# Optimization experiments

Measured on AMD Instinct MI355X. Metric: run time of the kernel, lower is better.

The kernel has to match this reference:

```python
import jax, jax.numpy as jnp
import numpy as np

# Collage decoder constants (from init_kwargs)
RES = 256          # config.data_res
C = 3              # collage_width
RH = RW = 8        # range patch size
DH = DW = 64       # domain patch size
N_DH = RES // DH   # 4 domain patches per side
N_D = N_DH * N_DH  # 16 domain patches
N_RH = RES // RH   # 32 range patches per side
N_R = N_RH * N_RH  # 1024 range patches
HF = DH // RH      # 8: pooling factor domain->range size
STEPS = 10


def setup_inputs() -> dict:
    key = jax.random.key(0)
    k1, k2, k3 = jax.random.split(key, 3)
    patch_emb = jax.random.normal(k1, (8, RH, RW, 256), dtype=jnp.float32)
    # get_1x1(theta_width): 1x1 conv == channel matmul, weight (256, 147456)
    w_theta = jax.random.normal(k2, (256, N_R * 3 * N_D * C), dtype=jnp.float32) * 0.01
    b_theta = jax.random.normal(k3, (N_R * 3 * N_D * C,), dtype=jnp.float32) * 0.01
    return {"patch_emb": patch_emb, "w_theta": w_theta, "b_theta": b_theta}


def reference(patch_emb, w_theta, b_theta):
    bs = patch_emb.shape[0]
    # patch_to_theta (1x1 conv) then avg_pool over full spatial extent -> (bs, theta_width)
    theta = jnp.einsum('bhwk,kt->bhwt', patch_emb, w_theta) + b_theta
    theta = theta.mean(axis=(1, 2))
    theta = theta.reshape(bs, 3 * N_R, N_D, C)
    mul, add, mix = jnp.split(theta, 3, axis=1)       # each (bs, N_R, N_D, C)
    mix = jax.nn.softmax(mix, axis=1)                 # softmax over range-patch axis (axis=1)
    mul = jnp.tanh(mul) * mix
    add = jnp.tanh(add) * mix
    add_sum = add.sum(axis=2)                         # (bs, N_R, C)

    iterate = jnp.zeros((bs, RES, RES, C), dtype=patch_emb.dtype)
    for _ in range(STEPS):
        # partition_img: gather domain patches -> (bs, N_D, DH, DW, C)
        d = iterate.reshape(bs, N_DH, DH, N_DH, DW, C)
        d = d.transpose(0, 1, 3, 2, 4, 5).reshape(bs, N_D, DH, DW, C)
        # reduce: mean-pool each domain patch down to range size (bs, N_D, RH, RW, C)
        d = d.reshape(bs, N_D, RH, HF, RW, HF, C).mean(axis=(3, 5))
        # affine combine: soft collage links every range to every domain
        out = jnp.einsum('brdc,bdhwc->brhwc', mul, d) + add_sum[:, :, None, None, :]
        iterate = out.reshape(bs, N_RH, N_RH, RH, RW, C)
        iterate = iterate.transpose(0, 1, 3, 2, 4, 5).reshape(bs, RES, RES, C)
    return iterate
```

## Files before the change

kernel.cpp:

```cpp
#include <hip/hip_runtime.h>
#include <math.h>

#define T_COLS 147456
#define BS 8
#define NU 49152

#define OFF_ME      0
#define OFF_THETA   2048
#define OFF_MULP    (OFF_THETA + BS*T_COLS)
#define OFF_ADDSUM  (OFF_MULP + 8*3*1024*16)
#define OFF_Q       (OFF_ADDSUM + 8*3*1024)

__device__ __forceinline__ float tanh_fast(float x) {
    float e = __expf(2.f * x);
    return 1.f - 2.f * __builtin_amdgcn_rcpf(e + 1.f);
}

__global__ __launch_bounds__(1024) void k1_mean(const float* __restrict__ pe,
                                                float* __restrict__ me) {
    int b = blockIdx.x;
    int k = threadIdx.x & 255, qd = threadIdx.x >> 8;
    const float* p = pe + (size_t)b * 16384 + qd * 4096 + k;
    float s = 0.f;
#pragma unroll
    for (int i = 0; i < 16; i++) s += p[i * 256];
    __shared__ float part[4][256];
    part[qd][k] = s;
    __syncthreads();
    if (threadIdx.x < 256) {
        float v = part[0][k] + part[1][k] + part[2][k] + part[3][k];
        me[k * 8 + b] = v * (1.f / 64.f);
    }
}

__global__ __launch_bounds__(192) void k2_gemm(const float* __restrict__ w,
                                               const float* __restrict__ bt,
                                               const float* __restrict__ me,
                                               float* __restrict__ tt) {
    __shared__ __align__(16) float lme[2048];
    __shared__ float lt[8][192];
    int tid = threadIdx.x;
    for (int i = tid; i < 2048; i += 192) lme[i] = me[i];
    __syncthreads();

    int t = blockIdx.x * 192 + tid;
    const float* wp = w + t;
    float bv = bt[t];

    float acc[8];
#pragma unroll
    for (int b = 0; b < 8; b++) acc[b] = 0.f;

#pragma unroll 32
    for (int k = 0; k < 256; k++) {
        float wv = wp[(size_t)k * T_COLS];
        const float4* m4 = reinterpret_cast<const float4*>(&lme[k * 8]);
        float4 m0 = m4[0], m1 = m4[1];
        acc[0] += m0.x * wv;
        acc[1] += m0.y * wv;
        acc[2] += m0.z * wv;
        acc[3] += m0.w * wv;
        acc[4] += m1.x * wv;
        acc[5] += m1.y * wv;
        acc[6] += m1.z * wv;
        acc[7] += m1.w * wv;
    }
#pragma unroll
    for (int b = 0; b < 8; b++) lt[b][tid] = acc[b] + bv;
    __syncthreads();

    int u0 = blockIdx.x * 64;
    int j = tid & 63;
    int c = tid >> 6;
#pragma unroll
    for (int b = 0; b < 8; b++) {
        float v = lt[b][j * 3 + c];
        tt[(size_t)(b * 3 + c) * NU + u0 + j] = v;
    }
}

#define MVL_STRIDE 1028
__global__ __launch_bounds__(1024) void kC(const float* __restrict__ tt,
                                           float* __restrict__ mulp,
                                           float* __restrict__ addsum,
                                           float* __restrict__ q) {
    int bc = blockIdx.x;
    int r = threadIdx.x;
    int lane = r & 63, wv = r >> 6;
    const float4* base = reinterpret_cast<const float4*>(tt + (size_t)bc * NU);

    __shared__ float redm[16 * 16];
    __shared__ float gm[16], ginv[16];
    __shared__ float mvl[16 * MVL_STRIDE];
    __shared__ float sred[1024];
    __shared__ float Ash[256];
    __shared__ float svl[16], pl[16];

    float mx[16];
    {
        float4 x0 = base[8192 + r * 4 + 0];
        float4 x1 = base[8192 + r * 4 + 1];
        float4 x2 = base[8192 + r * 4 + 2];
        float4 x3 = base[8192 + r * 4 + 3];
        mx[0] = x0.x; mx[1] = x0.y; mx[2] = x0.z; mx[3] = x0.w;
        mx[4] = x1.x; mx[5] = x1.y; mx[6] = x1.z; mx[7] = x1.w;
        mx[8] = x2.x; mx[9] = x2.y; mx[10] = x2.z; mx[11] = x2.w;
        mx[12] = x3.x; mx[13] = x3.y; mx[14] = x3.z; mx[15] = x3.w;
    }
    {
        float wred[16];
#pragma unroll
        for (int d = 0; d < 16; d++) wred[d] = mx[d];
#pragma unroll
        for (int m = 32; m > 0; m >>= 1)
#pragma unroll
            for (int d = 0; d < 16; d++)
                wred[d] = fmaxf(wred[d], __shfl_xor(wred[d], m));
        if (lane == 0) {
#pragma unroll
            for (int d = 0; d < 16; d++) redm[wv * 16 + d] = wred[d];
        }
    }
    __syncthreads();
    if (r < 16) {
        float m = -1e30f;
#pragma unroll
        for (int w = 0; w < 16; w++) m = fmaxf(m, redm[w * 16 + r]);
        gm[r] = m;
    }
    __syncthreads();

    {
        float wred[16];
#pragma unroll
        for (int d = 0; d < 16; d++) {
            mx[d] = __expf(mx[d] - gm[d]);
            wred[d] = mx[d];
        }
#pragma unroll
        for (int m = 32; m > 0; m >>= 1)
#pragma unroll
            for (int d = 0; d < 16; d++)
                wred[d] += __shfl_xor(wred[d], m);
        if (lane == 0) {
#pragma unroll
            for (int d = 0; d < 16; d++) redm[wv * 16 + d] = wred[d];
        }
    }
    __syncthreads();
    if (r < 16) {
        float s = 0.f;
#pragma unroll
        for (int w = 0; w < 16; w++) s += redm[w * 16 + r];
        ginv[r] = 1.f / s;
    }
    __syncthreads();
#pragma unroll
    for (int d = 0; d < 16; d++) mx[d] *= ginv[d];

    float asum = 0.f;
    {
        float4 a0 = base[4096 + r * 4 + 0];
        float4 a1 = base[4096 + r * 4 + 1];
        float4 a2 = base[4096 + r * 4 + 2];
        float4 a3 = base[4096 + r * 4 + 3];
        float av[16];
        av[0] = a0.x; av[1] = a0.y; av[2] = a0.z; av[3] = a0.w;
        av[4] = a1.x; av[5] = a1.y; av[6] = a1.z; av[7] = a1.w;
        av[8] = a2.x; av[9] = a2.y; av[10] = a2.z; av[11] = a2.w;
        av[12] = a3.x; av[13] = a3.y; av[14] = a3.z; av[15] = a3.w;
#pragma unroll
        for (int d = 0; d < 16; d++) asum += tanh_fast(av[d]) * mx[d];
    }
    addsum[(size_t)bc * 1024 + r] = asum;
    sred[r] = asum;

    float mv[16];
    {
        float4 m0 = base[r * 4 + 0];
        float4 m1 = base[r * 4 + 1];
        float4 m2 = base[r * 4 + 2];
        float4 m3 = base[r * 4 + 3];
        mv[0] = m0.x; mv[1] = m0.y; mv[2] = m0.z; mv[3] = m0.w;
        mv[4] = m1.x; mv[5] = m1.y; mv[6] = m1.z; mv[7] = m1.w;
        mv[8] = m2.x; mv[9] = m2.y; mv[10] = m2.z; mv[11] = m2.w;
        mv[12] = m3.x; mv[13] = m3.y; mv[14] = m3.z; mv[15] = m3.w;
#pragma unroll
        for (int d = 0; d < 16; d++) mv[d] = tanh_fast(mv[d]) * mx[d];
    }
    {
        float4* mp = reinterpret_cast<float4*>(&mulp[((size_t)bc * 1024 + r) * 16]);
        mp[0] = make_float4(mv[0], mv[1], mv[2], mv[3]);
        mp[1] = make_float4(mv[4], mv[5], mv[6], mv[7]);
        mp[2] = make_float4(mv[8], mv[9], mv[10], mv[11]);
        mp[3] = make_float4(mv[12], mv[13], mv[14], mv[15]);
    }
#pragma unroll
    for (int d = 0; d < 16; d++) mvl[d * MVL_STRIDE + r] = mv[d];
    __syncthreads();

    if (r < 256) {
        int dd = r >> 4, d = r & 15;
        int di = dd >> 2, dj = dd & 3;
        const float* bse = &mvl[d * MVL_STRIDE + di * 256 + dj * 8];
        float s = 0.f;
        for (int a = 0; a < 8; a++) {
#pragma unroll
            for (int e = 0; e < 8; e++) s += bse[a * 32 + e];
        }
        Ash[r] = s * (1.f / 64.f);
    }
    if (r < 16) {
        int di = r >> 2, dj = r & 3;
        float s = 0.f;
        for (int a = 0; a < 8; a++)
#pragma unroll
            for (int e = 0; e < 8; e++) s += sred[di * 256 + a * 32 + dj * 8 + e];
        svl[r] = s * (1.f / 64.f);
    }
    __syncthreads();

    if (r < 64) {
        int d2 = r & 15;
        float arow[16];
#pragma unroll
        for (int d = 0; d < 16; d++) arow[d] = Ash[d2 * 16 + d];
        float sv = svl[d2];
        float pd = 0.f;
        for (int it = 0; it < 8; it++) {
            float x = sv;
#pragma unroll
            for (int d = 0; d < 16; d++) x += arow[d] * __shfl(pd, d, 16);
            pd = x;
        }
        if (r < 16) pl[r] = pd;
    }
    __syncthreads();

    {
        float x = asum;
#pragma unroll
        for (int d = 0; d < 16; d++) x += mv[d] * pl[d];
        q[(size_t)bc * 1024 + r] = x;
    }
}

__global__ __launch_bounds__(512) void k5_final(const float* __restrict__ mulp,
                                                const float* __restrict__ addsum,
                                                const float* __restrict__ q,
                                                float* __restrict__ out) {
    int blk = blockIdx.x;
    int b = blk >> 5, ri = blk & 31;
    int tid = threadIdx.x;
    __shared__ float ql[3072];
    for (int i = tid; i < 3072; i += 512) ql[i] = q[(size_t)b * 3072 + i];
    __syncthreads();

    int h = tid >> 6;
    int rj = (tid >> 1) & 31;
    int wh = tid & 1;
    int r = ri * 32 + rj;

    float mr[3][16];
    float as[3];
#pragma unroll
    for (int c = 0; c < 3; c++) {
        const float4* mp4 = reinterpret_cast<const float4*>(
            &mulp[((size_t)(b * 3 + c) * 1024 + r) * 16]);
        float4 v0 = mp4[0], v1 = mp4[1], v2 = mp4[2], v3 = mp4[3];
        mr[c][0] = v0.x; mr[c][1] = v0.y; mr[c][2] = v0.z; mr[c][3] = v0.w;
        mr[c][4] = v1.x; mr[c][5] = v1.y; mr[c][6] = v1.z; mr[c][7] = v1.w;
        mr[c][8] = v2.x; mr[c][9] = v2.y; mr[c][10] = v2.z; mr[c][11] = v2.w;
        mr[c][12] = v3.x; mr[c][13] = v3.y; mr[c][14] = v3.z; mr[c][15] = v3.w;
        as[c] = addsum[(size_t)(b * 3 + c) * 1024 + r];
    }

    float acc[3][4];
#pragma unroll
    for (int c = 0; c < 3; c++)
#pragma unroll
        for (int w = 0; w < 4; w++) acc[c][w] = as[c];

#pragma unroll
    for (int di = 0; di < 4; di++) {
        int qrow = (di * 8 + h) * 32;
#pragma unroll
        for (int dj = 0; dj < 4; dj++) {
#pragma unroll
            for (int c = 0; c < 3; c++) {
                float m = mr[c][di * 4 + dj];
                const float* qb = &ql[c * 1024 + qrow + dj * 8 + wh * 4];
                acc[c][0] += m * qb[0];
                acc[c][1] += m * qb[1];
                acc[c][2] += m * qb[2];
                acc[c][3] += m * qb[3];
            }
        }
    }

    int i = ri * 8 + h;
    int j0 = rj * 8 + wh * 4;
    float4* ob = reinterpret_cast<float4*>(
        &out[((size_t)(b * 256 + i) * 256 + j0) * 3]);
    ob[0] = make_float4(acc[0][0], acc[1][0], acc[2][0], acc[0][1]);
    ob[1] = make_float4(acc[1][1], acc[2][1], acc[0][2], acc[1][2]);
    ob[2] = make_float4(acc[2][2], acc[0][3], acc[1][3], acc[2][3]);
}

extern "C" void kernel_launch(void* const* d_in, const int* in_sizes, int n_in,
                              void* d_out, int out_size, void* d_ws, size_t ws_size,
                              hipStream_t stream) {
    const float* pe = (const float*)d_in[0];
    const float* w  = (const float*)d_in[1];
    const float* bt = (const float*)d_in[2];
    float* ws = (float*)d_ws;

    float* me     = ws + OFF_ME;
    float* tt     = ws + OFF_THETA;
    float* mulp   = ws + OFF_MULP;
    float* addsum = ws + OFF_ADDSUM;
    float* q      = ws + OFF_Q;
    float* out = (float*)d_out;

    k1_mean<<<8, 1024, 0, stream>>>(pe, me);
    k2_gemm<<<T_COLS / 192, 192, 0, stream>>>(w, bt, me, tt);
    kC<<<24, 1024, 0, stream>>>(tt, mulp, addsum, q);
    k5_final<<<256, 512, 0, stream>>>(mulp, addsum, q, out);
}
```

Before: 60.77 us.

## Fuse GEMM, softmax and final stages into one persistent kernel with grid barriers

Replaces the three launches after the mean kernel with a single persistent kernel of 768 blocks. Atomic-counter grid barriers separate the theta GEMM, the per-channel softmax/fixed-point stage (now 256 threads handling 4 rows each) and the final image assembly. The aim is to remove kernel launch gaps and tail effects between the stages. The risks are spin-wait cost, a deadlock if 768 blocks are not all co-resident (checked only through an occupancy query), and the middle stage running on just 24 blocks while the rest idle.

```diff
diff --git a/kernel.cpp b/kernel.cpp
--- a/kernel.cpp
+++ b/kernel.cpp
@@ -2,22 +2,35 @@
 #include <math.h>
 
 #define T_COLS 147456
-#define BS 8
 #define NU 49152
 
 #define OFF_ME      0
 #define OFF_THETA   2048
-#define OFF_MULP    (OFF_THETA + BS*T_COLS)
+#define OFF_MULP    (OFF_THETA + 8*T_COLS)
 #define OFF_ADDSUM  (OFF_MULP + 8*3*1024*16)
 #define OFF_Q       (OFF_ADDSUM + 8*3*1024)
+#define OFF_BAR     (OFF_Q + 8*3*1024)
 
 __device__ __forceinline__ float tanh_fast(float x) {
     float e = __expf(2.f * x);
     return 1.f - 2.f * __builtin_amdgcn_rcpf(e + 1.f);
 }
 
-__global__ __launch_bounds__(1024) void k1_mean(const float* __restrict__ pe,
-                                                float* __restrict__ me) {
+__device__ __forceinline__ void gridbar(unsigned int* bar, unsigned int target) {
+    __syncthreads();
+    if (threadIdx.x == 0) {
+        __threadfence();
+        atomicAdd(bar, 1u);
+        while (atomicAdd(bar, 0u) < target) __builtin_amdgcn_s_sleep(2);
+        __threadfence();
+    }
+    __syncthreads();
+}
+
+__global__ __launch_bounds__(1024) void k1z(const float* __restrict__ pe,
+                                            float* __restrict__ me,
+                                            unsigned int* __restrict__ bar) {
+    if (blockIdx.x == 0 && threadIdx.x < 2) bar[threadIdx.x] = 0u;
     int b = blockIdx.x;
     int k = threadIdx.x & 255, qd = threadIdx.x >> 8;
     const float* p = pe + (size_t)b * 16384 + qd * 4096 + k;
@@ -30,6 +43,276 @@
     if (threadIdx.x < 256) {
         float v = part[0][k] + part[1][k] + part[2][k] + part[3][k];
         me[k * 8 + b] = v * (1.f / 64.f);
+    }
+}
+
+__global__ __launch_bounds__(256, 3) void mega(
+        const float* __restrict__ w, const float* __restrict__ bt,
+        const float* __restrict__ me, float* __restrict__ tt,
+        float* __restrict__ mulp, float* __restrict__ addsum,
+        float* __restrict__ q, float* __restrict__ out,
+        unsigned int* __restrict__ bar) {
+    const int bid = blockIdx.x;
+    const int tid = threadIdx.x;
+
+    __shared__ __align__(16) float lme[2048];
+    __shared__ float lt[8][192];
+    __shared__ __align__(16) float red[256 * 16];
+    __shared__ float sred[256];
+    __shared__ float Ash[256];
+    __shared__ float gmax[16], ginv[16], svl[16], pl[16];
+    __shared__ float ql3[3072];
+
+    {
+        for (int i = tid; i < 2048; i += 256) lme[i] = me[i];
+        __syncthreads();
+        if (tid < 192) {
+            int t = bid * 192 + tid;
+            const float* wp = w + t;
+            float acc[8];
+#pragma unroll
+            for (int b = 0; b < 8; b++) acc[b] = 0.f;
+#pragma unroll 16
+            for (int k = 0; k < 256; k++) {
+                float wv = wp[(size_t)k * T_COLS];
+                const float4* m4 = reinterpret_cast<const float4*>(&lme[k * 8]);
+                float4 m0 = m4[0], m1 = m4[1];
+                acc[0] += m0.x * wv; acc[1] += m0.y * wv;
+                acc[2] += m0.z * wv; acc[3] += m0.w * wv;
+                acc[4] += m1.x * wv; acc[5] += m1.y * wv;
+                acc[6] += m1.z * wv; acc[7] += m1.w * wv;
+            }
+            float bv = bt[t];
+#pragma unroll
+            for (int b = 0; b < 8; b++) lt[b][tid] = acc[b] + bv;
+        }
+        __syncthreads();
+        if (tid < 192) {
+            int u0 = bid * 64;
+            int j = tid & 63;
+            int c = tid >> 6;
+#pragma unroll
+            for (int b = 0; b < 8; b++)
+                tt[(size_t)(b * 3 + c) * NU + u0 + j] = lt[b][j * 3 + c];
+        }
+    }
+    gridbar(&bar[0], 768);
+
+    if (bid < 24) {
+        const int bc = bid;
+        const float4* base4 = reinterpret_cast<const float4*>(tt + (size_t)bc * NU);
+        const int r0 = tid * 4;
+        const int lane = tid & 63, wvi = tid >> 6;
+
+        float sm[4][16];
+        float lmax[16];
+#pragma unroll
+        for (int d = 0; d < 16; d++) lmax[d] = -1e30f;
+#pragma unroll
+        for (int i = 0; i < 4; i++) {
+            float4 x0 = base4[(2048 + r0 + i) * 4 + 0];
+            float4 x1 = base4[(2048 + r0 + i) * 4 + 1];
+            float4 x2 = base4[(2048 + r0 + i) * 4 + 2];
+            float4 x3 = base4[(2048 + r0 + i) * 4 + 3];
+            sm[i][0] = x0.x; sm[i][1] = x0.y; sm[i][2] = x0.z; sm[i][3] = x0.w;
+            sm[i][4] = x1.x; sm[i][5] = x1.y; sm[i][6] = x1.z; sm[i][7] = x1.w;
+            sm[i][8] = x2.x; sm[i][9] = x2.y; sm[i][10] = x2.z; sm[i][11] = x2.w;
+            sm[i][12] = x3.x; sm[i][13] = x3.y; sm[i][14] = x3.z; sm[i][15] = x3.w;
+#pragma unroll
+            for (int d = 0; d < 16; d++) lmax[d] = fmaxf(lmax[d], sm[i][d]);
+        }
+#pragma unroll
+        for (int m = 32; m > 0; m >>= 1)
+#pragma unroll
+            for (int d = 0; d < 16; d++)
+                lmax[d] = fmaxf(lmax[d], __shfl_xor(lmax[d], m));
+        if (lane == 0) {
+#pragma unroll
+            for (int d = 0; d < 16; d++) red[wvi * 16 + d] = lmax[d];
+        }
+        __syncthreads();
+        if (tid < 16)
+            gmax[tid] = fmaxf(fmaxf(red[tid], red[16 + tid]),
+                              fmaxf(red[32 + tid], red[48 + tid]));
+        __syncthreads();
+
+        float lsum[16];
+#pragma unroll
+        for (int d = 0; d < 16; d++) lsum[d] = 0.f;
+#pragma unroll
+        for (int i = 0; i < 4; i++)
+#pragma unroll
+            for (int d = 0; d < 16; d++) {
+                sm[i][d] = __expf(sm[i][d] - gmax[d]);
+                lsum[d] += sm[i][d];
+            }
+#pragma unroll
+        for (int m = 32; m > 0; m >>= 1)
+#pragma unroll
+            for (int d = 0; d < 16; d++) lsum[d] += __shfl_xor(lsum[d], m);
+        if (lane == 0) {
+#pragma unroll
+            for (int d = 0; d < 16; d++) red[wvi * 16 + d] = lsum[d];
+        }
+        __syncthreads();
+        if (tid < 16)
+            ginv[tid] = 1.f / (red[tid] + red[16 + tid] + red[32 + tid] + red[48 + tid]);
+        __syncthreads();
+#pragma unroll
+        for (int i = 0; i < 4; i++)
+#pragma unroll
+            for (int d = 0; d < 16; d++) sm[i][d] *= ginv[d];
+
+        float asum[4];
+#pragma unroll
+        for (int i = 0; i < 4; i++) {
+            float4 a0 = base4[(1024 + r0 + i) * 4 + 0];
+            float4 a1 = base4[(1024 + r0 + i) * 4 + 1];
+            float4 a2 = base4[(1024 + r0 + i) * 4 + 2];
+            float4 a3 = base4[(1024 + r0 + i) * 4 + 3];
+            float av[16];
+            av[0] = a0.x; av[1] = a0.y; av[2] = a0.z; av[3] = a0.w;
+            av[4] = a1.x; av[5] = a1.y; av[6] = a1.z; av[7] = a1.w;
+            av[8] = a2.x; av[9] = a2.y; av[10] = a2.z; av[11] = a2.w;
+            av[12] = a3.x; av[13] = a3.y; av[14] = a3.z; av[15] = a3.w;
+            float s = 0.f;
+#pragma unroll
+            for (int d = 0; d < 16; d++) s += tanh_fast(av[d]) * sm[i][d];
+            asum[i] = s;
+            addsum[(size_t)bc * 1024 + r0 + i] = s;
+        }
+        sred[tid] = asum[0] + asum[1] + asum[2] + asum[3];
+
+#pragma unroll
+        for (int i = 0; i < 4; i++) {
+            float4 m0 = base4[(r0 + i) * 4 + 0];
+            float4 m1 = base4[(r0 + i) * 4 + 1];
+            float4 m2 = base4[(r0 + i) * 4 + 2];
+            float4 m3 = base4[(r0 + i) * 4 + 3];
+            float mvv[16];
+            mvv[0] = m0.x; mvv[1] = m0.y; mvv[2] = m0.z; mvv[3] = m0.w;
+            mvv[4] = m1.x; mvv[5] = m1.y; mvv[6] = m1.z; mvv[7] = m1.w;
+            mvv[8] = m2.x; mvv[9] = m2.y; mvv[10] = m2.z; mvv[11] = m2.w;
+            mvv[12] = m3.x; mvv[13] = m3.y; mvv[14] = m3.z; mvv[15] = m3.w;
+#pragma unroll
+            for (int d = 0; d < 16; d++) sm[i][d] = tanh_fast(mvv[d]) * sm[i][d];
+            float4* mp = reinterpret_cast<float4*>(&mulp[((size_t)bc * 1024 + r0 + i) * 16]);
+            mp[0] = make_float4(sm[i][0], sm[i][1], sm[i][2], sm[i][3]);
+            mp[1] = make_float4(sm[i][4], sm[i][5], sm[i][6], sm[i][7]);
+            mp[2] = make_float4(sm[i][8], sm[i][9], sm[i][10], sm[i][11]);
+            mp[3] = make_float4(sm[i][12], sm[i][13], sm[i][14], sm[i][15]);
+        }
+
+#pragma unroll
+        for (int d = 0; d < 16; d++)
+            red[tid * 16 + d] = sm[0][d] + sm[1][d] + sm[2][d] + sm[3][d];
+        __syncthreads();
+        {
+            int dd = tid >> 4, d = tid & 15;
+            int di = dd >> 2, dj = dd & 3;
+            float s = 0.f;
+#pragma unroll
+            for (int a = 0; a < 8; a++) {
+                int t0 = di * 64 + a * 8 + dj * 2;
+                s += red[t0 * 16 + d] + red[(t0 + 1) * 16 + d];
+            }
+            Ash[tid] = s * (1.f / 64.f);
+        }
+        if (tid < 16) {
+            int di = tid >> 2, dj = tid & 3;
+            float s = 0.f;
+#pragma unroll
+            for (int a = 0; a < 8; a++) {
+                int t0 = di * 64 + a * 8 + dj * 2;
+                s += sred[t0] + sred[t0 + 1];
+            }
+            svl[tid] = s * (1.f / 64.f);
+        }
+        __syncthreads();
+
+        if (tid < 64) {
+            int d2 = tid & 15;
+            float arow[16];
+#pragma unroll
+            for (int d = 0; d < 16; d++) arow[d] = Ash[d2 * 16 + d];
+            float sv = svl[d2];
+            float pd = 0.f;
+            for (int it = 0; it < 8; it++) {
+                float x = sv;
+#pragma unroll
+                for (int d = 0; d < 16; d++) x += arow[d] * __shfl(pd, d, 16);
+                pd = x;
+            }
+            if (tid < 16) pl[tid] = pd;
+        }
+        __syncthreads();
+
+#pragma unroll
+        for (int i = 0; i < 4; i++) {
+            float x = asum[i];
+#pragma unroll
+            for (int d = 0; d < 16; d++) x += sm[i][d] * pl[d];
+            q[(size_t)bc * 1024 + r0 + i] = x;
+        }
+    }
+    gridbar(&bar[1], 768);
+
+    if (bid < 256) {
+        int b = bid >> 5, ri = bid & 31;
+        for (int i = tid; i < 3072; i += 256) ql3[i] = q[(size_t)b * 3072 + i];
+        __syncthreads();
+
+        int h0 = tid >> 6;
+        int rj = (tid >> 1) & 31;
+        int wh = tid & 1;
+        int r = ri * 32 + rj;
+
+        float mr[3][16];
+        float as[3];
+#pragma unroll
+        for (int c = 0; c < 3; c++) {
+            const float4* mp4 = reinterpret_cast<const float4*>(
+                &mulp[((size_t)(b * 3 + c) * 1024 + r) * 16]);
+            float4 v0 = mp4[0], v1 = mp4[1], v2 = mp4[2], v3 = mp4[3];
+            mr[c][0] = v0.x; mr[c][1] = v0.y; mr[c][2] = v0.z; mr[c][3] = v0.w;
+            mr[c][4] = v1.x; mr[c][5] = v1.y; mr[c][6] = v1.z; mr[c][7] = v1.w;
+            mr[c][8] = v2.x; mr[c][9] = v2.y; mr[c][10] = v2.z; mr[c][11] = v2.w;
+            mr[c][12] = v3.x; mr[c][13] = v3.y; mr[c][14] = v3.z; mr[c][15] = v3.w;
+            as[c] = addsum[(size_t)(b * 3 + c) * 1024 + r];
+        }
+
+#pragma unroll
+        for (int hh = 0; hh < 2; hh++) {
+            int h = h0 + hh * 4;
+            float acc[3][4];
+#pragma unroll
+            for (int c = 0; c < 3; c++)
+#pragma unroll
+                for (int x = 0; x < 4; x++) acc[c][x] = as[c];
+#pragma unroll
+            for (int di = 0; di < 4; di++) {
+                int qrow = (di * 8 + h) * 32;
+#pragma unroll
+                for (int dj = 0; dj < 4; dj++) {
+#pragma unroll
+                    for (int c = 0; c < 3; c++) {
+                        float m = mr[c][di * 4 + dj];
+                        const float* qb = &ql3[c * 1024 + qrow + dj * 8 + wh * 4];
+                        acc[c][0] += m * qb[0];
+                        acc[c][1] += m * qb[1];
+                        acc[c][2] += m * qb[2];
+                        acc[c][3] += m * qb[3];
+                    }
+                }
+            }
+            int i = ri * 8 + h;
+            int j0 = rj * 8 + wh * 4;
+            float4* ob = reinterpret_cast<float4*>(
+                &out[((size_t)(b * 256 + i) * 256 + j0) * 3]);
+            ob[0] = make_float4(acc[0][0], acc[1][0], acc[2][0], acc[0][1]);
+            ob[1] = make_float4(acc[1][1], acc[2][1], acc[0][2], acc[1][2]);
+            ob[2] = make_float4(acc[2][2], acc[0][3], acc[1][3], acc[2][3]);
+        }
     }
 }
 
@@ -42,41 +325,31 @@
     int tid = threadIdx.x;
     for (int i = tid; i < 2048; i += 192) lme[i] = me[i];
     __syncthreads();
-
     int t = blockIdx.x * 192 + tid;
     const float* wp = w + t;
     float bv = bt[t];
-
     float acc[8];
 #pragma unroll
     for (int b = 0; b < 8; b++) acc[b] = 0.f;
-
 #pragma unroll 32
     for (int k = 0; k < 256; k++) {
         float wv = wp[(size_t)k * T_COLS];
         const float4* m4 = reinterpret_cast<const float4*>(&lme[k * 8]);
         float4 m0 = m4[0], m1 = m4[1];
-        acc[0] += m0.x * wv;
-        acc[1] += m0.y * wv;
-        acc[2] += m0.z * wv;
-        acc[3] += m0.w * wv;
-        acc[4] += m1.x * wv;
-        acc[5] += m1.y * wv;
-        acc[6] += m1.z * wv;
-        acc[7] += m1.w * wv;
+        acc[0] += m0.x * wv; acc[1] += m0.y * wv;
+        acc[2] += m0.z * wv; acc[3] += m0.w * wv;
+        acc[4] += m1.x * wv; acc[5] += m1.y * wv;
+        acc[6] += m1.z * wv; acc[7] += m1.w * wv;
     }
 #pragma unroll
     for (int b = 0; b < 8; b++) lt[b][tid] = acc[b] + bv;
     __syncthreads();
-
     int u0 = blockIdx.x * 64;
     int j = tid & 63;
     int c = tid >> 6;
 #pragma unroll
-    for (int b = 0; b < 8; b++) {
-        float v = lt[b][j * 3 + c];
-        tt[(size_t)(b * 3 + c) * NU + u0 + j] = v;
-    }
+    for (int b = 0; b < 8; b++)
+        tt[(size_t)(b * 3 + c) * NU + u0 + j] = lt[b][j * 3 + c];
 }
 
 #define MVL_STRIDE 1028
@@ -88,20 +361,16 @@
     int r = threadIdx.x;
     int lane = r & 63, wv = r >> 6;
     const float4* base = reinterpret_cast<const float4*>(tt + (size_t)bc * NU);
-
     __shared__ float redm[16 * 16];
     __shared__ float gm[16], ginv[16];
     __shared__ float mvl[16 * MVL_STRIDE];
     __shared__ float sred[1024];
     __shared__ float Ash[256];
     __shared__ float svl[16], pl[16];
-
     float mx[16];
     {
-        float4 x0 = base[8192 + r * 4 + 0];
-        float4 x1 = base[8192 + r * 4 + 1];
-        float4 x2 = base[8192 + r * 4 + 2];
-        float4 x3 = base[8192 + r * 4 + 3];
+        float4 x0 = base[8192 + r * 4 + 0], x1 = base[8192 + r * 4 + 1];
+        float4 x2 = base[8192 + r * 4 + 2], x3 = base[8192 + r * 4 + 3];
         mx[0] = x0.x; mx[1] = x0.y; mx[2] = x0.z; mx[3] = x0.w;
         mx[4] = x1.x; mx[5] = x1.y; mx[6] = x1.z; mx[7] = x1.w;
         mx[8] = x2.x; mx[9] = x2.y; mx[10] = x2.z; mx[11] = x2.w;
@@ -116,10 +385,9 @@
 #pragma unroll
             for (int d = 0; d < 16; d++)
                 wred[d] = fmaxf(wred[d], __shfl_xor(wred[d], m));
-        if (lane == 0) {
+        if (lane == 0)
 #pragma unroll
             for (int d = 0; d < 16; d++) redm[wv * 16 + d] = wred[d];
-        }
     }
     __syncthreads();
     if (r < 16) {
@@ -129,23 +397,17 @@
         gm[r] = m;
     }
     __syncthreads();
-
     {
         float wred[16];
 #pragma unroll
-        for (int d = 0; d < 16; d++) {
-            mx[d] = __expf(mx[d] - gm[d]);
-            wred[d] = mx[d];
-        }
+        for (int d = 0; d < 16; d++) { mx[d] = __expf(mx[d] - gm[d]); wred[d] = mx[d]; }
 #pragma unroll
         for (int m = 32; m > 0; m >>= 1)
 #pragma unroll
-            for (int d = 0; d < 16; d++)
-                wred[d] += __shfl_xor(wred[d], m);
-        if (lane == 0) {
+            for (int d = 0; d < 16; d++) wred[d] += __shfl_xor(wred[d], m);
+        if (lane == 0)
 #pragma unroll
             for (int d = 0; d < 16; d++) redm[wv * 16 + d] = wred[d];
-        }
     }
     __syncthreads();
     if (r < 16) {
@@ -157,13 +419,10 @@
     __syncthreads();
 #pragma unroll
     for (int d = 0; d < 16; d++) mx[d] *= ginv[d];
-
     float asum = 0.f;
     {
-        float4 a0 = base[4096 + r * 4 + 0];
-        float4 a1 = base[4096 + r * 4 + 1];
-        float4 a2 = base[4096 + r * 4 + 2];
-        float4 a3 = base[4096 + r * 4 + 3];
+        float4 a0 = base[4096 + r * 4 + 0], a1 = base[4096 + r * 4 + 1];
+        float4 a2 = base[4096 + r * 4 + 2], a3 = base[4096 + r * 4 + 3];
         float av[16];
         av[0] = a0.x; av[1] = a0.y; av[2] = a0.z; av[3] = a0.w;
         av[4] = a1.x; av[5] = a1.y; av[6] = a1.z; av[7] = a1.w;
@@ -174,13 +433,10 @@
     }
     addsum[(size_t)bc * 1024 + r] = asum;
     sred[r] = asum;
-
     float mv[16];
     {
-        float4 m0 = base[r * 4 + 0];
-        float4 m1 = base[r * 4 + 1];
-        float4 m2 = base[r * 4 + 2];
-        float4 m3 = base[r * 4 + 3];
+        float4 m0 = base[r * 4 + 0], m1 = base[r * 4 + 1];
+        float4 m2 = base[r * 4 + 2], m3 = base[r * 4 + 3];
         mv[0] = m0.x; mv[1] = m0.y; mv[2] = m0.z; mv[3] = m0.w;
         mv[4] = m1.x; mv[5] = m1.y; mv[6] = m1.z; mv[7] = m1.w;
         mv[8] = m2.x; mv[9] = m2.y; mv[10] = m2.z; mv[11] = m2.w;
@@ -198,16 +454,14 @@
 #pragma unroll
     for (int d = 0; d < 16; d++) mvl[d * MVL_STRIDE + r] = mv[d];
     __syncthreads();
-
     if (r < 256) {
         int dd = r >> 4, d = r & 15;
         int di = dd >> 2, dj = dd & 3;
         const float* bse = &mvl[d * MVL_STRIDE + di * 256 + dj * 8];
         float s = 0.f;
-        for (int a = 0; a < 8; a++) {
+        for (int a = 0; a < 8; a++)
 #pragma unroll
             for (int e = 0; e < 8; e++) s += bse[a * 32 + e];
-        }
         Ash[r] = s * (1.f / 64.f);
     }
     if (r < 16) {
@@ -219,7 +473,6 @@
         svl[r] = s * (1.f / 64.f);
     }
     __syncthreads();
-
     if (r < 64) {
         int d2 = r & 15;
         float arow[16];
@@ -236,7 +489,6 @@
         if (r < 16) pl[r] = pd;
     }
     __syncthreads();
-
     {
         float x = asum;
 #pragma unroll
@@ -255,12 +507,10 @@
     __shared__ float ql[3072];
     for (int i = tid; i < 3072; i += 512) ql[i] = q[(size_t)b * 3072 + i];
     __syncthreads();
-
     int h = tid >> 6;
     int rj = (tid >> 1) & 31;
     int wh = tid & 1;
     int r = ri * 32 + rj;
-
     float mr[3][16];
     float as[3];
 #pragma unroll
@@ -274,13 +524,11 @@
         mr[c][12] = v3.x; mr[c][13] = v3.y; mr[c][14] = v3.z; mr[c][15] = v3.w;
         as[c] = addsum[(size_t)(b * 3 + c) * 1024 + r];
     }
-
     float acc[3][4];
 #pragma unroll
     for (int c = 0; c < 3; c++)
 #pragma unroll
         for (int w = 0; w < 4; w++) acc[c][w] = as[c];
-
 #pragma unroll
     for (int di = 0; di < 4; di++) {
         int qrow = (di * 8 + h) * 32;
@@ -297,7 +545,6 @@
             }
         }
     }
-
     int i = ri * 8 + h;
     int j0 = rj * 8 + wh * 4;
     float4* ob = reinterpret_cast<float4*>(
@@ -320,10 +567,18 @@
     float* mulp   = ws + OFF_MULP;
     float* addsum = ws + OFF_ADDSUM;
     float* q      = ws + OFF_Q;
+    unsigned int* bar = (unsigned int*)(ws + OFF_BAR);
     float* out = (float*)d_out;
 
-    k1_mean<<<8, 1024, 0, stream>>>(pe, me);
-    k2_gemm<<<T_COLS / 192, 192, 0, stream>>>(w, bt, me, tt);
-    kC<<<24, 1024, 0, stream>>>(tt, mulp, addsum, q);
-    k5_final<<<256, 512, 0, stream>>>(mulp, addsum, q, out);
-}
+    int occ = 0;
+    (void)hipOccupancyMaxActiveBlocksPerMultiprocessor(&occ, mega, 256, 0);
+
+    k1z<<<8, 1024, 0, stream>>>(pe, me, bar);
+    if (occ >= 3) {
+        mega<<<768, 256, 0, stream>>>(w, bt, me, tt, mulp, addsum, q, out, bar);
+    } else {
+        k2_gemm<<<T_COLS / 192, 192, 0, stream>>>(w, bt, me, tt);
+        kC<<<24, 1024, 0, stream>>>(tt, mulp, addsum, q);
+        k5_final<<<256, 512, 0, stream>>>(mulp, addsum, q, out);
+    }
+}
```

Result: no change. 60.76 us (-0.0%).

## Split the theta GEMM along K into four partial passes plus a reduction kernel

Applied to the files above, without the earlier changes.

The weight-streaming GEMM is split into four K-slices, so four times as many blocks are launched, each covering 64 of the 256 input channels and writing partial sums to workspace. A new reduction kernel adds the partials and the bias, then does the transposed scatter into the theta buffer that the GEMM used to do. The goal is more memory-level parallelism while streaming the large weight matrix, which the original 768-block grid likely underused. The cost is an extra kernel launch and extra workspace traffic for the partial sums, and it assumes the workspace is large enough for the new partial buffer.

```diff
diff --git a/kernel.cpp b/kernel.cpp
--- a/kernel.cpp
+++ b/kernel.cpp
@@ -2,14 +2,15 @@
 #include <math.h>
 
 #define T_COLS 147456
-#define BS 8
 #define NU 49152
+#define KSPLIT 4
 
 #define OFF_ME      0
 #define OFF_THETA   2048
-#define OFF_MULP    (OFF_THETA + BS*T_COLS)
+#define OFF_MULP    (OFF_THETA + 8*T_COLS)
 #define OFF_ADDSUM  (OFF_MULP + 8*3*1024*16)
 #define OFF_Q       (OFF_ADDSUM + 8*3*1024)
+#define OFF_PART    (OFF_Q + 8*3*1024)
 
 __device__ __forceinline__ float tanh_fast(float x) {
     float e = __expf(2.f * x);
@@ -34,25 +35,26 @@
 }
 
 __global__ __launch_bounds__(192) void k2_gemm(const float* __restrict__ w,
-                                               const float* __restrict__ bt,
                                                const float* __restrict__ me,
-                                               float* __restrict__ tt) {
+                                               float* __restrict__ part) {
     __shared__ __align__(16) float lme[2048];
-    __shared__ float lt[8][192];
     int tid = threadIdx.x;
     for (int i = tid; i < 2048; i += 192) lme[i] = me[i];
     __syncthreads();
 
-    int t = blockIdx.x * 192 + tid;
+    int bid = blockIdx.x;
+    int s = bid & 3, cw = bid >> 2;
+    int t = cw * 192 + tid;
     const float* wp = w + t;
-    float bv = bt[t];
+    const int k0 = s * 64;
 
     float acc[8];
 #pragma unroll
     for (int b = 0; b < 8; b++) acc[b] = 0.f;
 
 #pragma unroll 32
-    for (int k = 0; k < 256; k++) {
+    for (int kk = 0; kk < 64; kk++) {
+        int k = k0 + kk;
         float wv = wp[(size_t)k * T_COLS];
         const float4* m4 = reinterpret_cast<const float4*>(&lme[k * 8]);
         float4 m0 = m4[0], m1 = m4[1];
@@ -66,7 +68,29 @@
         acc[7] += m1.w * wv;
     }
 #pragma unroll
-    for (int b = 0; b < 8; b++) lt[b][tid] = acc[b] + bv;
+    for (int b = 0; b < 8; b++)
+        part[(size_t)(s * 8 + b) * T_COLS + t] = acc[b];
+}
+
+__global__ __launch_bounds__(192) void kR(const float* __restrict__ part,
+                                          const float* __restrict__ bt,
+                                          float* __restrict__ tt) {
+    __shared__ float lt[8][192];
+    int tid = threadIdx.x;
+    int t = blockIdx.x * 192 + tid;
+    float bv = bt[t];
+
+    float acc[8];
+#pragma unroll
+    for (int b = 0; b < 8; b++) acc[b] = bv;
+#pragma unroll
+    for (int s = 0; s < KSPLIT; s++) {
+#pragma unroll
+        for (int b = 0; b < 8; b++)
+            acc[b] += part[(size_t)(s * 8 + b) * T_COLS + t];
+    }
+#pragma unroll
+    for (int b = 0; b < 8; b++) lt[b][tid] = acc[b];
     __syncthreads();
 
     int u0 = blockIdx.x * 64;
@@ -320,10 +344,12 @@
     float* mulp   = ws + OFF_MULP;
     float* addsum = ws + OFF_ADDSUM;
     float* q      = ws + OFF_Q;
+    float* part   = ws + OFF_PART;
     float* out = (float*)d_out;
 
     k1_mean<<<8, 1024, 0, stream>>>(pe, me);
-    k2_gemm<<<T_COLS / 192, 192, 0, stream>>>(w, bt, me, tt);
+    k2_gemm<<<768 * KSPLIT, 192, 0, stream>>>(w, me, part);
+    kR<<<T_COLS / 192, 192, 0, stream>>>(part, bt, tt);
     kC<<<24, 1024, 0, stream>>>(tt, mulp, addsum, q);
     k5_final<<<256, 512, 0, stream>>>(mulp, addsum, q, out);
 }
```

Result: slower. 71.05 us (+16.9%).
